# Kernel tuning notes

Hardware: AMD Instinct MI355X
Metric: run time of the kernel (lower is better)

Reference implementation:

```python
import jax, jax.numpy as jnp
import numpy as np

H1, H2, T, D_IN, NUM_CLASSES = 128, 64, 128, 2, 11


def _lstm(xs, W_ih, W_hh):
    """Single-layer LSTM, bias=False, PyTorch gate order (i,f,g,o).
    xs: [B,T,D]; W_ih: [4H,D]; W_hh: [4H,H] -> returns hidden seq [B,T,H]."""
    B = xs.shape[0]
    H = W_hh.shape[1]
    # Precompute input projections for all timesteps at once: [B,T,4H]
    xg = jnp.einsum('btd,gd->btg', xs, W_ih)
    W_hh_T = W_hh.T  # [H,4H]

    def step(carry, xg_t):
        h, c = carry
        g = xg_t + h @ W_hh_T  # [B,4H]
        i, f, gg, o = jnp.split(g, 4, axis=-1)
        i = jax.nn.sigmoid(i)
        f = jax.nn.sigmoid(f)
        gg = jnp.tanh(gg)
        o = jax.nn.sigmoid(o)
        c = f * c + i * gg
        h = o * jnp.tanh(c)
        return (h, c), h

    h0 = jnp.zeros((B, H), xs.dtype)
    (_, _), hs = jax.lax.scan(step, (h0, h0), jnp.swapaxes(xg, 0, 1))
    return jnp.swapaxes(hs, 0, 1)  # [B,T,H]


def setup_inputs() -> dict:
    key = jax.random.key(0)
    ks = jax.random.split(key, 7)
    B = 2048
    s1 = 1.0 / np.sqrt(H1)
    s2 = 1.0 / np.sqrt(H2)
    sf = 1.0 / np.sqrt(T * H2)
    return {
        'x': jax.random.normal(ks[0], (B, D_IN, T), dtype=jnp.float32),
        'W_ih1': jax.random.uniform(ks[1], (4 * H1, D_IN), jnp.float32, -s1, s1),
        'W_hh1': jax.random.uniform(ks[2], (4 * H1, H1), jnp.float32, -s1, s1),
        'W_ih2': jax.random.uniform(ks[3], (4 * H2, H1), jnp.float32, -s2, s2),
        'W_hh2': jax.random.uniform(ks[4], (4 * H2, H2), jnp.float32, -s2, s2),
        'W_fc': jax.random.uniform(ks[5], (NUM_CLASSES, T * H2), jnp.float32, -sf, sf),
        'b_fc': jax.random.uniform(ks[6], (NUM_CLASSES,), jnp.float32, -sf, sf),
    }


def reference(x, W_ih1, W_hh1, W_ih2, W_hh2, W_fc, b_fc):
    xs = jnp.swapaxes(x, 2, 1)          # [B,T,2]
    h1 = _lstm(xs, W_ih1, W_hh1)        # [B,T,128]
    h2 = _lstm(h1, W_ih2, W_hh2)        # [B,T,64]
    flat = h2.reshape(h2.shape[0], -1)  # [B,8192]
    return flat @ W_fc.T + b_fc         # [B,11]
```

## Files before the change

### kernel.cpp

```cpp
#include <hip/hip_runtime.h>

#define TSTEPS 128
#define NCLS 11
#define BTILE 8
#define WTOT 114688
#define WFCF 131072

typedef float f32x2 __attribute__((ext_vector_type(2)));
typedef float f32x4 __attribute__((ext_vector_type(4)));

__device__ __forceinline__ float rcpf_(float x) { return __builtin_amdgcn_rcpf(x); }
__device__ __forceinline__ float sigm(float x) { return rcpf_(1.0f + __expf(-x)); }
__device__ __forceinline__ float tanhf_(float x) { return 1.0f - 2.0f * rcpf_(__expf(2.0f * x) + 1.0f); }

__device__ __forceinline__ void pk_lo(f32x2& acc, f32x2 w, f32x2 h) {
    asm("v_pk_fma_f32 %0, %1, %2, %0 op_sel:[0,0,0] op_sel_hi:[1,0,1]"
        : "+v"(acc) : "v"(w), "v"(h));
}
__device__ __forceinline__ void pk_hi(f32x2& acc, f32x2 w, f32x2 h) {
    asm("v_pk_fma_f32 %0, %1, %2, %0 op_sel:[0,1,0] op_sel_hi:[1,1,1]"
        : "+v"(acc) : "v"(w), "v"(h));
}
#define SV2(v, a, b) __builtin_shufflevector((v), (v), (a), (b))

template <int CTRL>
__device__ __forceinline__ float dppf(float x) {
    return __int_as_float(__builtin_amdgcn_update_dpp(
        0, __float_as_int(x), CTRL, 0xF, 0xF, true));
}
template <int CTRL>
__device__ __forceinline__ f32x2 dpp2(f32x2 v) {
    f32x2 r;
    r.x = dppf<CTRL>(v.x);
    r.y = dppf<CTRL>(v.y);
    return r;
}

__global__ void prep_weights(const float* __restrict__ Whh1,
                             const float* __restrict__ Wih2,
                             const float* __restrict__ Whh2,
                             const float* __restrict__ Wfc,
                             float* __restrict__ ws, int packFc) {
    int idx = blockIdx.x * blockDim.x + threadIdx.x;
    if (idx < WTOT) {
        int idx4 = idx >> 2, kk = idx & 3;
        int oct = idx4 / 224;
        int r4 = idx4 - oct * 224;
        int chunk = r4 >> 3;
        int tid = oct * 8 + (r4 & 7);
        float v;
        if (chunk < 16) {
            int p = chunk >> 3, rem = chunk & 7, j = rem >> 1, h = rem & 1;
            int s = tid & 7, d = tid >> 3;
            int gate = 2 * p + (kk & 1);
            int col = 4 * (s + 8 * j) + 2 * h + (kk >> 1);
            v = Whh1[(gate * 128 + d) * 128 + col];
        } else {
            int c2 = chunk - 16;
            int p = c2 / 6, rem = c2 - 6 * p, j = rem >> 1, h = rem & 1;
            int s2 = tid & 15, d2 = tid >> 4;
            int gate = 2 * p + (kk & 1);
            int col = 4 * (s2 + 16 * j) + 2 * h + (kk >> 1);
            int row = gate * 64 + d2;
            v = (col < 128) ? Wih2[row * 128 + col] : Whh2[row * 64 + (col - 128)];
        }
        ws[idx] = v;
    } else if (packFc && idx < WTOT + WFCF) {
        int r = idx - WTOT;
        int t = r >> 10;
        int rem = r & 1023;
        int d2 = rem >> 4, slot = rem & 15;
        float v = 0.0f;
        if (slot < 6) v = Wfc[slot * 8192 + t * 64 + d2];
        else if (slot >= 8 && slot <= 12) v = Wfc[(slot - 2) * 8192 + t * 64 + d2];
        ws[idx] = v;
    }
}

__global__ __attribute__((amdgpu_flat_work_group_size(1024, 1024),
                          amdgpu_waves_per_eu(4, 4)))
void lstm_fused_t(const float* __restrict__ x, const float* __restrict__ Wih1,
                  const float* __restrict__ Wfc, const float* __restrict__ bfc,
                  const float* __restrict__ ws, float* __restrict__ out, int packed) {

    __shared__ __align__(16) float lx[BTILE][2 * TSTEPS + 4];
    __shared__ __align__(16) float lh1[2][BTILE][128];
    __shared__ __align__(16) float lh2[2][BTILE][64];
    __shared__ __align__(16) float4 lwih4[2][128];
    __shared__ float lfacc[1024][7];
    __shared__ float fpart[16][BTILE][NCLS];

    const int tid = threadIdx.x;
    const int b0 = blockIdx.x * BTILE;

    for (int i = tid; i < BTILE * 2 * TSTEPS; i += 1024)
        lx[i >> 8][i & 255] = x[b0 * 256 + i];
    for (int i = tid; i < 2 * BTILE * 128; i += 1024)
        ((float*)lh1)[i] = 0.0f;
    if (tid < 2 * BTILE * 64) ((float*)lh2)[tid] = 0.0f;
    for (int i = tid; i < 1024 * 7; i += 1024)
        ((float*)lfacc)[i] = 0.0f;
    if (tid < 128) {
        const float2* wp = (const float2*)Wih1;
        const float2 ri = wp[tid], rf = wp[128 + tid], rg = wp[256 + tid], ro = wp[384 + tid];
        lwih4[0][tid] = make_float4(ri.x, ri.y, rf.x, rf.y);
        lwih4[1][tid] = make_float4(rg.x, rg.y, ro.x, ro.y);
    }

    const int d  = tid >> 3;
    const int s  = tid & 7;
    const int d2 = tid >> 4;
    const int s2 = tid & 15;
    const bool lowh = (s2 < 8);

    const f32x4* __restrict__ wqt = (const f32x4*)ws + ((tid >> 3) * 224 + (tid & 7));
    const float* __restrict__ wfcPk = ws + WTOT + ((d2 << 4) + (lowh ? 0 : 8));

    float c1 = 0.0f, c2v = 0.0f;

    __syncthreads();

#pragma unroll 1
    for (int t = 0; t < TSTEPS; ++t) {
        const int tb = t & 1;
        const int xb = tb ^ 1;
        const bool f4 = (s & 4) != 0;
        const bool f2 = (s & 2) != 0;
        const bool f1 = (s & 1) != 0;

        f32x2 rif;
        {
            f32x2 AB[8];
#pragma unroll
            for (int b = 0; b < 8; ++b) AB[b] = (f32x2){0.0f, 0.0f};
#pragma unroll
            for (int j = 0; j < 4; ++j) {
                const f32x4 c0 = wqt[(2 * j) * 8];
                const f32x4 ch = wqt[(2 * j + 1) * 8];
                const int ko = 4 * (s + 8 * j);
#pragma unroll
                for (int b = 0; b < 8; ++b) {
                    const f32x4 h4 = *(const f32x4*)&lh1[xb][b][ko];
                    const f32x2 h01 = SV2(h4, 0, 1), h23 = SV2(h4, 2, 3);
                    pk_lo(AB[b], SV2(c0, 0, 1), h01);
                    pk_hi(AB[b], SV2(c0, 2, 3), h01);
                    pk_lo(AB[b], SV2(ch, 0, 1), h23);
                    pk_hi(AB[b], SV2(ch, 2, 3), h23);
                }
            }
            f32x2 Aa[4];
#pragma unroll
            for (int i = 0; i < 4; ++i)
                Aa[i] = (f4 ? AB[i+4] : AB[i]) + dpp2<0x141>(f4 ? AB[i] : AB[i+4]);
            f32x2 Ba[2];
#pragma unroll
            for (int i = 0; i < 2; ++i)
                Ba[i] = (f2 ? Aa[i+2] : Aa[i]) + dpp2<0x4E>(f2 ? Aa[i] : Aa[i+2]);
            rif = (f1 ? Ba[1] : Ba[0]) + dpp2<0xB1>(f1 ? Ba[0] : Ba[1]);
        }
        __builtin_amdgcn_sched_barrier(0);

        f32x2 rgo;
        {
            f32x2 AB[8];
#pragma unroll
            for (int b = 0; b < 8; ++b) AB[b] = (f32x2){0.0f, 0.0f};
#pragma unroll
            for (int j = 0; j < 4; ++j) {
                const f32x4 c0 = wqt[(8 + 2 * j) * 8];
                const f32x4 ch = wqt[(9 + 2 * j) * 8];
                const int ko = 4 * (s + 8 * j);
#pragma unroll
                for (int b = 0; b < 8; ++b) {
                    const f32x4 h4 = *(const f32x4*)&lh1[xb][b][ko];
                    const f32x2 h01 = SV2(h4, 0, 1), h23 = SV2(h4, 2, 3);
                    pk_lo(AB[b], SV2(c0, 0, 1), h01);
                    pk_hi(AB[b], SV2(c0, 2, 3), h01);
                    pk_lo(AB[b], SV2(ch, 0, 1), h23);
                    pk_hi(AB[b], SV2(ch, 2, 3), h23);
                }
            }
            f32x2 Aa[4];
#pragma unroll
            for (int i = 0; i < 4; ++i)
                Aa[i] = (f4 ? AB[i+4] : AB[i]) + dpp2<0x141>(f4 ? AB[i] : AB[i+4]);
            f32x2 Ba[2];
#pragma unroll
            for (int i = 0; i < 2; ++i)
                Ba[i] = (f2 ? Aa[i+2] : Aa[i]) + dpp2<0x4E>(f2 ? Aa[i] : Aa[i+2]);
            rgo = (f1 ? Ba[1] : Ba[0]) + dpp2<0xB1>(f1 ? Ba[0] : Ba[1]);
        }
        __builtin_amdgcn_sched_barrier(0);

        int zr; asm volatile("v_mov_b32 %0, 0" : "=v"(zr));
        const float4 wv0 = lwih4[0][d + zr];
        const float4 wv1 = lwih4[1][d + zr];
        const float x0 = lx[s][t], x1 = lx[s][TSTEPS + t];
        const float gi = rif.x + wv0.x * x0 + wv0.y * x1;
        const float gf = rif.y + wv0.z * x0 + wv0.w * x1;
        const float gg = rgo.x + wv1.x * x0 + wv1.y * x1;
        const float go = rgo.y + wv1.z * x0 + wv1.w * x1;
        const float i1 = sigm(gi), ff = sigm(gf), g1v = tanhf_(gg), o1 = sigm(go);
        c1 = ff * c1 + i1 * g1v;
        const float h1n = o1 * tanhf_(c1);

        lh1[tb][s][d] = h1n;
        __syncthreads();

        const bool g8 = (s2 & 8) != 0;
        const bool e4 = (s2 & 4) != 0;
        const bool e2 = (s2 & 2) != 0;
        const bool e1 = (s2 & 1) != 0;

        float DA, EA;
        {
            f32x2 AB[8];
#pragma unroll
            for (int b = 0; b < 8; ++b) AB[b] = (f32x2){0.0f, 0.0f};
#pragma unroll
            for (int j = 0; j < 3; ++j) {
                const f32x4 c0 = wqt[(16 + 2 * j) * 8];
                const f32x4 ch = wqt[(17 + 2 * j) * 8];
#pragma unroll
                for (int b = 0; b < 8; ++b) {
                    const f32x4 h4 = (j < 2)
                        ? *(const f32x4*)&lh1[tb][b][4 * s2 + 64 * j]
                        : *(const f32x4*)&lh2[xb][b][4 * s2];
                    const f32x2 h01 = SV2(h4, 0, 1), h23 = SV2(h4, 2, 3);
                    pk_lo(AB[b], SV2(c0, 0, 1), h01);
                    pk_hi(AB[b], SV2(c0, 2, 3), h01);
                    pk_lo(AB[b], SV2(ch, 0, 1), h23);
                    pk_hi(AB[b], SV2(ch, 2, 3), h23);
                }
            }
            float T[8];
#pragma unroll
            for (int b = 0; b < 8; ++b)
                T[b] = (g8 ? AB[b].y : AB[b].x) + dppf<0x128>(g8 ? AB[b].x : AB[b].y);
            float V[4];
#pragma unroll
            for (int i = 0; i < 4; ++i)
                V[i] = (e4 ? T[i+4] : T[i]) + dppf<0x141>(e4 ? T[i] : T[i+4]);
            float X[2];
#pragma unroll
            for (int i = 0; i < 2; ++i)
                X[i] = (e2 ? V[i+2] : V[i]) + dppf<0x4E>(e2 ? V[i] : V[i+2]);
            DA = (e1 ? X[1] : X[0]) + dppf<0xB1>(e1 ? X[0] : X[1]);
            EA = dppf<0x128>(DA);
        }
        __builtin_amdgcn_sched_barrier(0);

        float DB, EB;
        {
            f32x2 AB[8];
#pragma unroll
            for (int b = 0; b < 8; ++b) AB[b] = (f32x2){0.0f, 0.0f};
#pragma unroll
            for (int j = 0; j < 3; ++j) {
                const f32x4 c0 = wqt[(22 + 2 * j) * 8];
                const f32x4 ch = wqt[(23 + 2 * j) * 8];
#pragma unroll
                for (int b = 0; b < 8; ++b) {
                    const f32x4 h4 = (j < 2)
                        ? *(const f32x4*)&lh1[tb][b][4 * s2 + 64 * j]
                        : *(const f32x4*)&lh2[xb][b][4 * s2];
                    const f32x2 h01 = SV2(h4, 0, 1), h23 = SV2(h4, 2, 3);
                    pk_lo(AB[b], SV2(c0, 0, 1), h01);
                    pk_hi(AB[b], SV2(c0, 2, 3), h01);
                    pk_lo(AB[b], SV2(ch, 0, 1), h23);
                    pk_hi(AB[b], SV2(ch, 2, 3), h23);
                }
            }
            float T[8];
#pragma unroll
            for (int b = 0; b < 8; ++b)
                T[b] = (g8 ? AB[b].y : AB[b].x) + dppf<0x128>(g8 ? AB[b].x : AB[b].y);
            float V[4];
#pragma unroll
            for (int i = 0; i < 4; ++i)
                V[i] = (e4 ? T[i+4] : T[i]) + dppf<0x141>(e4 ? T[i] : T[i+4]);
            float X[2];
#pragma unroll
            for (int i = 0; i < 2; ++i)
                X[i] = (e2 ? V[i+2] : V[i]) + dppf<0x4E>(e2 ? V[i] : V[i+2]);
            DB = (e1 ? X[1] : X[0]) + dppf<0xB1>(e1 ? X[0] : X[1]);
            EB = dppf<0x128>(DB);
        }

        const float gi2 = lowh ? DA : EA;
        const float gf2 = lowh ? EA : DA;
        const float gg2 = lowh ? DB : EB;
        const float go2 = lowh ? EB : DB;
        const float i2 = sigm(gi2), f2g = sigm(gf2), g2v = tanhf_(gg2), o2 = sigm(go2);
        c2v = f2g * c2v + i2 * g2v;
        const float h2n = o2 * tanhf_(c2v);
        if (packed) {
            const float* fp = wfcPk + (t << 10);
            const float4 fa = *(const float4*)fp;
            const float2 fb = *(const float2*)(fp + 4);
            lfacc[tid][0] += h2n * fa.x;
            lfacc[tid][1] += h2n * fa.y;
            lfacc[tid][2] += h2n * fa.z;
            lfacc[tid][3] += h2n * fa.w;
            lfacc[tid][4] += h2n * fb.x;
            if (lowh) lfacc[tid][5] += h2n * fb.y;
        } else {
            const float* wfcp = Wfc + t * 64 + d2 + (lowh ? 0 : 6 * 8192);
            if (lowh) {
#pragma unroll
                for (int c = 0; c < 6; ++c) lfacc[tid][c] += h2n * wfcp[c * 8192];
            } else {
#pragma unroll
                for (int c = 0; c < 5; ++c) lfacc[tid][c] += h2n * wfcp[c * 8192];
            }
        }
        if (lowh) lh2[tb][s2][d2] = h2n;
    }

    float facc[6];
#pragma unroll
    for (int c = 0; c < 6; ++c) facc[c] = lfacc[tid][c];
#pragma unroll
    for (int c = 0; c < 6; ++c) {
        facc[c] += __shfl_xor(facc[c], 16);
        facc[c] += __shfl_xor(facc[c], 32);
    }
    const int wv = tid >> 6;
    if ((tid & 63) < 16) {
        const int bb = tid & 7;
        if ((tid & 15) < 8) {
#pragma unroll
            for (int c = 0; c < 6; ++c) fpart[wv][bb][c] = facc[c];
        } else {
#pragma unroll
            for (int c = 0; c < 5; ++c) fpart[wv][bb][6 + c] = facc[c];
        }
    }
    __syncthreads();
    if (tid < BTILE * NCLS) {
        const int bb = tid / NCLS, c = tid - bb * NCLS;
        float v = bfc[c];
#pragma unroll
        for (int w = 0; w < 16; ++w) v += fpart[w][bb][c];
        out[(b0 + bb) * NCLS + c] = v;
    }
}

extern "C" void kernel_launch(void* const* d_in, const int* in_sizes, int n_in,
                              void* d_out, int out_size, void* d_ws, size_t ws_size,
                              hipStream_t stream) {
    const float* x    = (const float*)d_in[0];
    const float* Wih1 = (const float*)d_in[1];
    const float* Whh1 = (const float*)d_in[2];
    const float* Wih2 = (const float*)d_in[3];
    const float* Whh2 = (const float*)d_in[4];
    const float* Wfc  = (const float*)d_in[5];
    const float* bfc  = (const float*)d_in[6];
    float* out = (float*)d_out;
    float* ws  = (float*)d_ws;

    const int packed = (ws_size >= (size_t)(WTOT + WFCF) * 4) ? 1 : 0;
    const int prep_elems = WTOT + (packed ? WFCF : 0);
    prep_weights<<<(prep_elems + 255) / 256, 256, 0, stream>>>(Whh1, Wih2, Whh2, Wfc, ws, packed);
    lstm_fused_t<<<256, 1024, 0, stream>>>(x, Wih1, Wfc, bfc, ws, out, packed);
}
```

Baseline: 1.252 ms.

## Fuse gate-pair matvecs to share LDS hidden-state loads across batch sub-blocks

Merges the separate i/f and g/o matvec passes for both LSTM layers into one loop that computes both gate pairs from each hidden-state LDS read. The batch is split into two sub-blocks of four so the accumulator count stays bounded. The reduction order is reorganised so the butterfly DPP reductions interleave per sub-block, and layer 2's reduction now runs on packed pairs before the final g8 lane split. This halves the LDS reads of h and uses fewer reduction shuffles, but raises register pressure and changes the instruction schedule.

```diff
diff --git a/kernel.cpp b/kernel.cpp
--- a/kernel.cpp
+++ b/kernel.cpp
@@ -108,7 +108,7 @@
     }
 
     const int d  = tid >> 3;
-    const int s  = tid & 7;
+    const int s_ = tid & 7;
     const int d2 = tid >> 4;
     const int s2 = tid & 15;
     const bool lowh = (s2 < 8);
@@ -124,78 +124,69 @@
     for (int t = 0; t < TSTEPS; ++t) {
         const int tb = t & 1;
         const int xb = tb ^ 1;
-        const bool f4 = (s & 4) != 0;
-        const bool f2 = (s & 2) != 0;
-        const bool f1 = (s & 1) != 0;
-
-        f32x2 rif;
+        const bool f4 = (s_ & 4) != 0;
+        const bool f2 = (s_ & 2) != 0;
+        const bool f1 = (s_ & 1) != 0;
+
+        f32x2 rif, rgo;
         {
-            f32x2 AB[8];
-#pragma unroll
-            for (int b = 0; b < 8; ++b) AB[b] = (f32x2){0.0f, 0.0f};
-#pragma unroll
-            for (int j = 0; j < 4; ++j) {
-                const f32x4 c0 = wqt[(2 * j) * 8];
-                const f32x4 ch = wqt[(2 * j + 1) * 8];
-                const int ko = 4 * (s + 8 * j);
-#pragma unroll
-                for (int b = 0; b < 8; ++b) {
-                    const f32x4 h4 = *(const f32x4*)&lh1[xb][b][ko];
-                    const f32x2 h01 = SV2(h4, 0, 1), h23 = SV2(h4, 2, 3);
-                    pk_lo(AB[b], SV2(c0, 0, 1), h01);
-                    pk_hi(AB[b], SV2(c0, 2, 3), h01);
-                    pk_lo(AB[b], SV2(ch, 0, 1), h23);
-                    pk_hi(AB[b], SV2(ch, 2, 3), h23);
-                }
+            f32x2 PifX, PgoX;
+#pragma unroll
+            for (int blk = 0; blk < 2; ++blk) {
+                f32x2 aif[2][2], ago[2][2];
+#pragma unroll
+                for (int k = 0; k < 2; ++k)
+#pragma unroll
+                    for (int i = 0; i < 2; ++i) {
+                        aif[k][i] = (f32x2){0.0f, 0.0f};
+                        ago[k][i] = (f32x2){0.0f, 0.0f};
+                    }
+#pragma unroll
+                for (int j = 0; j < 4; ++j) {
+                    const f32x4 wa0 = wqt[(2 * j) * 8];
+                    const f32x4 wa1 = wqt[(2 * j + 1) * 8];
+                    const f32x4 wb0 = wqt[(8 + 2 * j) * 8];
+                    const f32x4 wb1 = wqt[(9 + 2 * j) * 8];
+                    const int ko = 4 * (s_ + 8 * j);
+#pragma unroll
+                    for (int k = 0; k < 2; ++k)
+#pragma unroll
+                        for (int i = 0; i < 2; ++i) {
+                            const int b = 4 * k + i + 2 * blk;
+                            const f32x4 h4 = *(const f32x4*)&lh1[xb][b][ko];
+                            const f32x2 h01 = SV2(h4, 0, 1), h23 = SV2(h4, 2, 3);
+                            pk_lo(aif[k][i], SV2(wa0, 0, 1), h01);
+                            pk_hi(aif[k][i], SV2(wa0, 2, 3), h01);
+                            pk_lo(aif[k][i], SV2(wa1, 0, 1), h23);
+                            pk_hi(aif[k][i], SV2(wa1, 2, 3), h23);
+                            pk_lo(ago[k][i], SV2(wb0, 0, 1), h01);
+                            pk_hi(ago[k][i], SV2(wb0, 2, 3), h01);
+                            pk_lo(ago[k][i], SV2(wb1, 0, 1), h23);
+                            pk_hi(ago[k][i], SV2(wb1, 2, 3), h23);
+                        }
+                }
+                f32x2 Aif[2], Ago[2];
+#pragma unroll
+                for (int i = 0; i < 2; ++i) {
+                    Aif[i] = (f4 ? aif[1][i] : aif[0][i]) + dpp2<0x141>(f4 ? aif[0][i] : aif[1][i]);
+                    Ago[i] = (f4 ? ago[1][i] : ago[0][i]) + dpp2<0x141>(f4 ? ago[0][i] : ago[1][i]);
+                }
+                const f32x2 pif = (f1 ? Aif[1] : Aif[0]) + dpp2<0xB1>(f1 ? Aif[0] : Aif[1]);
+                const f32x2 pgo = (f1 ? Ago[1] : Ago[0]) + dpp2<0xB1>(f1 ? Ago[0] : Ago[1]);
+                if (blk == 0) {
+                    PifX = pif; PgoX = pgo;
+                } else {
+                    rif = (f2 ? pif : PifX) + dpp2<0x4E>(f2 ? PifX : pif);
+                    rgo = (f2 ? pgo : PgoX) + dpp2<0x4E>(f2 ? PgoX : pgo);
+                }
+                __builtin_amdgcn_sched_barrier(0);
             }
-            f32x2 Aa[4];
-#pragma unroll
-            for (int i = 0; i < 4; ++i)
-                Aa[i] = (f4 ? AB[i+4] : AB[i]) + dpp2<0x141>(f4 ? AB[i] : AB[i+4]);
-            f32x2 Ba[2];
-#pragma unroll
-            for (int i = 0; i < 2; ++i)
-                Ba[i] = (f2 ? Aa[i+2] : Aa[i]) + dpp2<0x4E>(f2 ? Aa[i] : Aa[i+2]);
-            rif = (f1 ? Ba[1] : Ba[0]) + dpp2<0xB1>(f1 ? Ba[0] : Ba[1]);
-        }
-        __builtin_amdgcn_sched_barrier(0);
-
-        f32x2 rgo;
-        {
-            f32x2 AB[8];
-#pragma unroll
-            for (int b = 0; b < 8; ++b) AB[b] = (f32x2){0.0f, 0.0f};
-#pragma unroll
-            for (int j = 0; j < 4; ++j) {
-                const f32x4 c0 = wqt[(8 + 2 * j) * 8];
-                const f32x4 ch = wqt[(9 + 2 * j) * 8];
-                const int ko = 4 * (s + 8 * j);
-#pragma unroll
-                for (int b = 0; b < 8; ++b) {
-                    const f32x4 h4 = *(const f32x4*)&lh1[xb][b][ko];
-                    const f32x2 h01 = SV2(h4, 0, 1), h23 = SV2(h4, 2, 3);
-                    pk_lo(AB[b], SV2(c0, 0, 1), h01);
-                    pk_hi(AB[b], SV2(c0, 2, 3), h01);
-                    pk_lo(AB[b], SV2(ch, 0, 1), h23);
-                    pk_hi(AB[b], SV2(ch, 2, 3), h23);
-                }
-            }
-            f32x2 Aa[4];
-#pragma unroll
-            for (int i = 0; i < 4; ++i)
-                Aa[i] = (f4 ? AB[i+4] : AB[i]) + dpp2<0x141>(f4 ? AB[i] : AB[i+4]);
-            f32x2 Ba[2];
-#pragma unroll
-            for (int i = 0; i < 2; ++i)
-                Ba[i] = (f2 ? Aa[i+2] : Aa[i]) + dpp2<0x4E>(f2 ? Aa[i] : Aa[i+2]);
-            rgo = (f1 ? Ba[1] : Ba[0]) + dpp2<0xB1>(f1 ? Ba[0] : Ba[1]);
-        }
-        __builtin_amdgcn_sched_barrier(0);
+        }
 
         int zr; asm volatile("v_mov_b32 %0, 0" : "=v"(zr));
         const float4 wv0 = lwih4[0][d + zr];
         const float4 wv1 = lwih4[1][d + zr];
-        const float x0 = lx[s][t], x1 = lx[s][TSTEPS + t];
+        const float x0 = lx[s_][t], x1 = lx[s_][TSTEPS + t];
         const float gi = rif.x + wv0.x * x0 + wv0.y * x1;
         const float gf = rif.y + wv0.z * x0 + wv0.w * x1;
         const float gg = rgo.x + wv1.x * x0 + wv1.y * x1;
@@ -204,7 +195,7 @@
         c1 = ff * c1 + i1 * g1v;
         const float h1n = o1 * tanhf_(c1);
 
-        lh1[tb][s][d] = h1n;
+        lh1[tb][s_][d] = h1n;
         __syncthreads();
 
         const bool g8 = (s2 & 8) != 0;
@@ -212,78 +203,63 @@
         const bool e2 = (s2 & 2) != 0;
         const bool e1 = (s2 & 1) != 0;
 
-        float DA, EA;
+        float DA, EA, DB, EB;
         {
-            f32x2 AB[8];
-#pragma unroll
-            for (int b = 0; b < 8; ++b) AB[b] = (f32x2){0.0f, 0.0f};
-#pragma unroll
-            for (int j = 0; j < 3; ++j) {
-                const f32x4 c0 = wqt[(16 + 2 * j) * 8];
-                const f32x4 ch = wqt[(17 + 2 * j) * 8];
-#pragma unroll
-                for (int b = 0; b < 8; ++b) {
-                    const f32x4 h4 = (j < 2)
-                        ? *(const f32x4*)&lh1[tb][b][4 * s2 + 64 * j]
-                        : *(const f32x4*)&lh2[xb][b][4 * s2];
-                    const f32x2 h01 = SV2(h4, 0, 1), h23 = SV2(h4, 2, 3);
-                    pk_lo(AB[b], SV2(c0, 0, 1), h01);
-                    pk_hi(AB[b], SV2(c0, 2, 3), h01);
-                    pk_lo(AB[b], SV2(ch, 0, 1), h23);
-                    pk_hi(AB[b], SV2(ch, 2, 3), h23);
-                }
+            f32x2 QifX, QgoX, Qif, Qgo;
+#pragma unroll
+            for (int blk = 0; blk < 2; ++blk) {
+                f32x2 uif[2][2], ugo[2][2];
+#pragma unroll
+                for (int k = 0; k < 2; ++k)
+#pragma unroll
+                    for (int i = 0; i < 2; ++i) {
+                        uif[k][i] = (f32x2){0.0f, 0.0f};
+                        ugo[k][i] = (f32x2){0.0f, 0.0f};
+                    }
+#pragma unroll
+                for (int j = 0; j < 3; ++j) {
+                    const f32x4 wa0 = wqt[(16 + 2 * j) * 8];
+                    const f32x4 wa1 = wqt[(17 + 2 * j) * 8];
+                    const f32x4 wb0 = wqt[(22 + 2 * j) * 8];
+                    const f32x4 wb1 = wqt[(23 + 2 * j) * 8];
+#pragma unroll
+                    for (int k = 0; k < 2; ++k)
+#pragma unroll
+                        for (int i = 0; i < 2; ++i) {
+                            const int b = 4 * k + i + 2 * blk;
+                            const f32x4 h4 = (j < 2)
+                                ? *(const f32x4*)&lh1[tb][b][4 * s2 + 64 * j]
+                                : *(const f32x4*)&lh2[xb][b][4 * s2];
+                            const f32x2 h01 = SV2(h4, 0, 1), h23 = SV2(h4, 2, 3);
+                            pk_lo(uif[k][i], SV2(wa0, 0, 1), h01);
+                            pk_hi(uif[k][i], SV2(wa0, 2, 3), h01);
+                            pk_lo(uif[k][i], SV2(wa1, 0, 1), h23);
+                            pk_hi(uif[k][i], SV2(wa1, 2, 3), h23);
+                            pk_lo(ugo[k][i], SV2(wb0, 0, 1), h01);
+                            pk_hi(ugo[k][i], SV2(wb0, 2, 3), h01);
+                            pk_lo(ugo[k][i], SV2(wb1, 0, 1), h23);
+                            pk_hi(ugo[k][i], SV2(wb1, 2, 3), h23);
+                        }
+                }
+                f32x2 U[2], V[2];
+#pragma unroll
+                for (int i = 0; i < 2; ++i) {
+                    U[i] = (e4 ? uif[1][i] : uif[0][i]) + dpp2<0x141>(e4 ? uif[0][i] : uif[1][i]);
+                    V[i] = (e4 ? ugo[1][i] : ugo[0][i]) + dpp2<0x141>(e4 ? ugo[0][i] : ugo[1][i]);
+                }
+                const f32x2 qif = (e1 ? U[1] : U[0]) + dpp2<0xB1>(e1 ? U[0] : U[1]);
+                const f32x2 qgo = (e1 ? V[1] : V[0]) + dpp2<0xB1>(e1 ? V[0] : V[1]);
+                if (blk == 0) {
+                    QifX = qif; QgoX = qgo;
+                } else {
+                    Qif = (e2 ? qif : QifX) + dpp2<0x4E>(e2 ? QifX : qif);
+                    Qgo = (e2 ? qgo : QgoX) + dpp2<0x4E>(e2 ? QgoX : qgo);
+                }
+                __builtin_amdgcn_sched_barrier(0);
             }
-            float T[8];
-#pragma unroll
-            for (int b = 0; b < 8; ++b)
-                T[b] = (g8 ? AB[b].y : AB[b].x) + dppf<0x128>(g8 ? AB[b].x : AB[b].y);
-            float V[4];
-#pragma unroll
-            for (int i = 0; i < 4; ++i)
-                V[i] = (e4 ? T[i+4] : T[i]) + dppf<0x141>(e4 ? T[i] : T[i+4]);
-            float X[2];
-#pragma unroll
-            for (int i = 0; i < 2; ++i)
-                X[i] = (e2 ? V[i+2] : V[i]) + dppf<0x4E>(e2 ? V[i] : V[i+2]);
-            DA = (e1 ? X[1] : X[0]) + dppf<0xB1>(e1 ? X[0] : X[1]);
+            DA = (g8 ? Qif.y : Qif.x) + dppf<0x128>(g8 ? Qif.x : Qif.y);
             EA = dppf<0x128>(DA);
-        }
-        __builtin_amdgcn_sched_barrier(0);
-
-        float DB, EB;
-        {
-            f32x2 AB[8];
-#pragma unroll
-            for (int b = 0; b < 8; ++b) AB[b] = (f32x2){0.0f, 0.0f};
-#pragma unroll
-            for (int j = 0; j < 3; ++j) {
-                const f32x4 c0 = wqt[(22 + 2 * j) * 8];
-                const f32x4 ch = wqt[(23 + 2 * j) * 8];
-#pragma unroll
-                for (int b = 0; b < 8; ++b) {
-                    const f32x4 h4 = (j < 2)
-                        ? *(const f32x4*)&lh1[tb][b][4 * s2 + 64 * j]
-                        : *(const f32x4*)&lh2[xb][b][4 * s2];
-                    const f32x2 h01 = SV2(h4, 0, 1), h23 = SV2(h4, 2, 3);
-                    pk_lo(AB[b], SV2(c0, 0, 1), h01);
-                    pk_hi(AB[b], SV2(c0, 2, 3), h01);
-                    pk_lo(AB[b], SV2(ch, 0, 1), h23);
-                    pk_hi(AB[b], SV2(ch, 2, 3), h23);
-                }
-            }
-            float T[8];
-#pragma unroll
-            for (int b = 0; b < 8; ++b)
-                T[b] = (g8 ? AB[b].y : AB[b].x) + dppf<0x128>(g8 ? AB[b].x : AB[b].y);
-            float V[4];
-#pragma unroll
-            for (int i = 0; i < 4; ++i)
-                V[i] = (e4 ? T[i+4] : T[i]) + dppf<0x141>(e4 ? T[i] : T[i+4]);
-            float X[2];
-#pragma unroll
-            for (int i = 0; i < 2; ++i)
-                X[i] = (e2 ? V[i+2] : V[i]) + dppf<0x4E>(e2 ? V[i] : V[i+2]);
-            DB = (e1 ? X[1] : X[0]) + dppf<0xB1>(e1 ? X[0] : X[1]);
+            DB = (g8 ? Qgo.y : Qgo.x) + dppf<0x128>(g8 ? Qgo.x : Qgo.y);
             EB = dppf<0x128>(DB);
         }
 
```

Measured after the change: 1.256 ms. No clear change (+0.3%).
